# Kernel tuning notes

Measured on AMD Instinct MI355X. Metric: run time of the kernel, lower is better.

The kernel has to match this reference:

```python
import jax, jax.numpy as jnp
import numpy as np

B, C, W = 8, 32, 64  # cube side W; input is [B, C, W*W, W] = flattened W^3 Hilbert cube


def setup_inputs() -> dict:
    key = jax.random.key(0)
    x = jax.random.normal(key, (B, C, W * W, W), dtype=jnp.float32)
    rng = np.random.default_rng(0)
    # Bijective index maps standing in for precomputed Hilbert-curve tables
    distance = jnp.asarray(rng.permutation(W ** 3), dtype=jnp.int32)        # 2D order -> 3D voxel order
    coordinate = jnp.asarray(rng.permutation((W // 2) ** 3), dtype=jnp.int32)  # pooled 3D -> 2D order
    return {"x": x, "distance": distance, "coordinate": coordinate}


def reference(x, distance, coordinate):
    b, c, h2d, w = x.shape            # h2d == w*w
    x_flat = x.reshape(b, c, -1)      # [B, C, W^3], 2D Hilbert order
    # inv_hilbert_permute_2d_to_3d: gather into 3D voxel order
    x_3d = jnp.take(x_flat, distance, axis=2).reshape(b, c, w, w, w)
    h = w // 2
    # MaxPool3d(kernel=2, stride=2) via reshape + max over 2x2x2 blocks
    pooled = x_3d.reshape(b, c, h, 2, h, 2, h, 2).max(axis=(3, 5, 7))  # [B, C, h, h, h]
    # hilbert_permute_3d_to_2d: gather back to 1D Hilbert order, view as 2D
    out = jnp.take(pooled.reshape(b, c, -1), coordinate, axis=2).reshape(b, c, -1, h)
    return out  # [B, C, (W/2)^2, W/2]
```

## Files before the change

kernel.cpp:

```cpp
#include <hip/hip_runtime.h>
#include <hip/hip_bf16.h>


#define N_VOX   262144
#define N_POOL  32768
#define N_BC    256

typedef float          f32x4 __attribute__((ext_vector_type(4)));
typedef unsigned int   u32x4 __attribute__((ext_vector_type(4)));
typedef unsigned short u16x4 __attribute__((ext_vector_type(4)));

__device__ __forceinline__ unsigned enc_f32(float f) {
    unsigned u = __float_as_uint(f);
    return u ^ (((int)u >> 31) | 0x80000000u);
}
__device__ __forceinline__ float dec_f32(unsigned u) {
    return __uint_as_float(u ^ (~((int)u >> 31) | 0x80000000u));
}

__global__ __launch_bounds__(256) void build_inv(const int* __restrict__ coordinate,
                                                 int* __restrict__ inv) {
    int j = blockIdx.x * 256 + threadIdx.x;
    inv[coordinate[j]] = j;
}

__global__ __launch_bounds__(256) void build_tgt(const int* __restrict__ distance,
                                                 const int* __restrict__ inv,
                                                 unsigned short* __restrict__ tgt) {
    int v  = blockIdx.x * 256 + threadIdx.x;
    int a0 = v >> 12, a1 = (v >> 6) & 63, a2 = v & 63;
    int p  = (a0 >> 1) * 1024 + (a1 >> 1) * 32 + (a2 >> 1);
    tgt[distance[v]] = (unsigned short)inv[p];
}

#define CH   4
#define NCH  (N_VOX / 4 / 1024 / CH)

__global__ __launch_bounds__(1024) void pool_scatter(const float* __restrict__ x,
                                                     const unsigned short* __restrict__ tgt,
                                                     float* __restrict__ out) {
    __shared__ unsigned int acc[N_POOL];
    const int tid = threadIdx.x;
    const int bc  = blockIdx.x;

    u32x4* a4i = (u32x4*)acc;
    const u32x4 z4 = {0u, 0u, 0u, 0u};
    #pragma unroll
    for (int k = 0; k < N_POOL / 4 / 1024; ++k)
        a4i[k * 1024 + tid] = z4;
    __syncthreads();

    const f32x4* x4 = (const f32x4*)(x + (size_t)bc * N_VOX);
    const u16x4* t4 = (const u16x4*)tgt;

    f32x4 xa[CH], xb[CH];
    u16x4 ta[CH], tb[CH];

#define LOADC(XV, TV, c)                                                     \
    {                                                                        \
        _Pragma("unroll")                                                    \
        for (int u = 0; u < CH; ++u) {                                       \
            int i = ((c) * CH + u) * 1024 + tid;                             \
            XV[u] = __builtin_nontemporal_load(&x4[i]);                      \
            TV[u] = t4[i];                                                   \
        }                                                                    \
    }

#define PROC(XV, TV)                                                         \
    {                                                                        \
        _Pragma("unroll")                                                    \
        for (int u = 0; u < CH; ++u) {                                       \
            atomicMax(&acc[TV[u].x], enc_f32(XV[u].x));                      \
            atomicMax(&acc[TV[u].y], enc_f32(XV[u].y));                      \
            atomicMax(&acc[TV[u].z], enc_f32(XV[u].z));                      \
            atomicMax(&acc[TV[u].w], enc_f32(XV[u].w));                      \
        }                                                                    \
    }

    LOADC(xa, ta, 0);
    for (int c = 0; c < NCH; c += 2) {
        LOADC(xb, tb, c + 1);
        PROC(xa, ta);
        if (c + 2 < NCH) LOADC(xa, ta, c + 2);
        PROC(xb, tb);
    }
    __syncthreads();

    const u32x4* a4 = (const u32x4*)acc;
    f32x4* o4 = (f32x4*)(out + (size_t)bc * N_POOL);
    #pragma unroll
    for (int k = 0; k < N_POOL / 4 / 1024; ++k) {
        int j4 = k * 1024 + tid;
        u32x4 a = a4[j4];
        f32x4 v;
        v.x = dec_f32(a.x);
        v.y = dec_f32(a.y);
        v.z = dec_f32(a.z);
        v.w = dec_f32(a.w);
        __builtin_nontemporal_store(v, &o4[j4]);
    }
}

__global__ __launch_bounds__(256) void pool_gather_fly(const float* __restrict__ x,
                                                       const int* __restrict__ distance,
                                                       const int* __restrict__ coordinate,
                                                       float* __restrict__ out) {
    int lb   = blockIdx.x;
    int xcd  = lb & 7;
    int q    = lb >> 3;
    int slab = q >> 7;
    int jb   = q & 127;
    int bc   = xcd + (slab << 3);
    int j    = (jb << 8) + threadIdx.x;

    int p  = coordinate[j];
    int a0 = p >> 10, a1 = (p >> 5) & 31, a2 = p & 31;
    int base = (a0 << 1) * 4096 + (a1 << 1) * 64 + (a2 << 1);

    const float* xb = x + (size_t)bc * N_VOX;
    float v = xb[distance[base]];
    v = fmaxf(v, xb[distance[base + 1]]);
    v = fmaxf(v, xb[distance[base + 64]]);
    v = fmaxf(v, xb[distance[base + 65]]);
    v = fmaxf(v, xb[distance[base + 4096]]);
    v = fmaxf(v, xb[distance[base + 4097]]);
    v = fmaxf(v, xb[distance[base + 4160]]);
    v = fmaxf(v, xb[distance[base + 4161]]);

    out[(size_t)bc * N_POOL + j] = v;
}

extern "C" void kernel_launch(void* const* d_in, const int* in_sizes, int n_in,
                              void* d_out, int out_size, void* d_ws, size_t ws_size,
                              hipStream_t stream) {
    const float* x          = (const float*)d_in[0];
    const int*   distance   = (const int*)d_in[1];
    const int*   coordinate = (const int*)d_in[2];
    float*       out        = (float*)d_out;

    const size_t need = (size_t)N_POOL * sizeof(int) + (size_t)N_VOX * sizeof(unsigned short);

    if (ws_size >= need) {
        int*            inv = (int*)d_ws;
        unsigned short* tgt = (unsigned short*)((char*)d_ws + (size_t)N_POOL * sizeof(int));
        build_inv<<<N_POOL / 256, 256, 0, stream>>>(coordinate, inv);
        build_tgt<<<N_VOX / 256, 256, 0, stream>>>(distance, inv, tgt);
        pool_scatter<<<N_BC, 1024, 0, stream>>>(x, tgt, out);
    } else {
        pool_gather_fly<<<N_BC * 128, 256, 0, stream>>>(x, distance, coordinate, out);
    }
}
```

Measured before the change: 61.34 us.

## Fuse index-table build into one kernel, overlap LDS zeroing with loads, widen chunks

Merges the two table-building kernels into one. Each pooled output index now writes its 8 source voxel targets directly, which removes one launch and the intermediate inverse array. In the scatter kernel, the first global loads are issued before the shared accumulator is zeroed. The chunk depth goes from 4 to 8 vectors per thread, and __syncthreads is replaced with an LDS-wait-plus-barrier. The deeper chunks increase register pressure, and the direct-scatter table build writes tgt with random short stores.

```diff
diff --git a/kernel.cpp b/kernel.cpp
--- a/kernel.cpp
+++ b/kernel.cpp
@@ -18,23 +18,30 @@
     return __uint_as_float(u ^ (~((int)u >> 31) | 0x80000000u));
 }
 
-__global__ __launch_bounds__(256) void build_inv(const int* __restrict__ coordinate,
-                                                 int* __restrict__ inv) {
+__global__ __launch_bounds__(256) void build_tgt_direct(const int* __restrict__ distance,
+                                                        const int* __restrict__ coordinate,
+                                                        unsigned short* __restrict__ tgt) {
     int j = blockIdx.x * 256 + threadIdx.x;
-    inv[coordinate[j]] = j;
+    int p = coordinate[j];
+    int base = ((p >> 10) << 1) * 4096 + (((p >> 5) & 31) << 1) * 64 + ((p & 31) << 1);
+    unsigned short js = (unsigned short)j;
+    tgt[distance[base]]        = js;
+    tgt[distance[base + 1]]    = js;
+    tgt[distance[base + 64]]   = js;
+    tgt[distance[base + 65]]   = js;
+    tgt[distance[base + 4096]] = js;
+    tgt[distance[base + 4097]] = js;
+    tgt[distance[base + 4160]] = js;
+    tgt[distance[base + 4161]] = js;
 }
 
-__global__ __launch_bounds__(256) void build_tgt(const int* __restrict__ distance,
-                                                 const int* __restrict__ inv,
-                                                 unsigned short* __restrict__ tgt) {
-    int v  = blockIdx.x * 256 + threadIdx.x;
-    int a0 = v >> 12, a1 = (v >> 6) & 63, a2 = v & 63;
-    int p  = (a0 >> 1) * 1024 + (a1 >> 1) * 32 + (a2 >> 1);
-    tgt[distance[v]] = (unsigned short)inv[p];
+#define CH   8
+#define NCH  (N_VOX / 4 / 1024 / CH)
+
+__device__ __forceinline__ void lds_barrier() {
+    asm volatile("s_waitcnt lgkmcnt(0)" ::: "memory");
+    __builtin_amdgcn_s_barrier();
 }
-
-#define CH   4
-#define NCH  (N_VOX / 4 / 1024 / CH)
 
 __global__ __launch_bounds__(1024) void pool_scatter(const float* __restrict__ x,
                                                      const unsigned short* __restrict__ tgt,
@@ -42,13 +49,6 @@
     __shared__ unsigned int acc[N_POOL];
     const int tid = threadIdx.x;
     const int bc  = blockIdx.x;
-
-    u32x4* a4i = (u32x4*)acc;
-    const u32x4 z4 = {0u, 0u, 0u, 0u};
-    #pragma unroll
-    for (int k = 0; k < N_POOL / 4 / 1024; ++k)
-        a4i[k * 1024 + tid] = z4;
-    __syncthreads();
 
     const f32x4* x4 = (const f32x4*)(x + (size_t)bc * N_VOX);
     const u16x4* t4 = (const u16x4*)tgt;
@@ -78,13 +78,21 @@
     }
 
     LOADC(xa, ta, 0);
+
+    u32x4* a4i = (u32x4*)acc;
+    const u32x4 z4 = {0u, 0u, 0u, 0u};
+    #pragma unroll
+    for (int k = 0; k < N_POOL / 4 / 1024; ++k)
+        a4i[k * 1024 + tid] = z4;
+    lds_barrier();
+
     for (int c = 0; c < NCH; c += 2) {
         LOADC(xb, tb, c + 1);
         PROC(xa, ta);
         if (c + 2 < NCH) LOADC(xa, ta, c + 2);
         PROC(xb, tb);
     }
-    __syncthreads();
+    lds_barrier();
 
     const u32x4* a4 = (const u32x4*)acc;
     f32x4* o4 = (f32x4*)(out + (size_t)bc * N_POOL);
@@ -138,13 +146,11 @@
     const int*   coordinate = (const int*)d_in[2];
     float*       out        = (float*)d_out;
 
-    const size_t need = (size_t)N_POOL * sizeof(int) + (size_t)N_VOX * sizeof(unsigned short);
+    const size_t need = (size_t)N_VOX * sizeof(unsigned short);
 
     if (ws_size >= need) {
-        int*            inv = (int*)d_ws;
-        unsigned short* tgt = (unsigned short*)((char*)d_ws + (size_t)N_POOL * sizeof(int));
-        build_inv<<<N_POOL / 256, 256, 0, stream>>>(coordinate, inv);
-        build_tgt<<<N_VOX / 256, 256, 0, stream>>>(distance, inv, tgt);
+        unsigned short* tgt = (unsigned short*)d_ws;
+        build_tgt_direct<<<N_POOL / 256, 256, 0, stream>>>(distance, coordinate, tgt);
         pool_scatter<<<N_BC, 1024, 0, stream>>>(x, tgt, out);
     } else {
         pool_gather_fly<<<N_BC * 128, 256, 0, stream>>>(x, distance, coordinate, out);
```

New measurement: 58.94 us. 1.04x faster.
